# Performance work log

Measured on AMD Instinct MI355X. Metric: run time of the kernel, lower is better.

The kernel has to match this reference:

```python
import jax, jax.numpy as jnp
import numpy as np

_FP8_DTYPE = jnp.float8_e4m3fn
_FP8_MAX = 448.0  # finfo(float8_e4m3fn).max


def setup_inputs() -> dict:
    key = jax.random.key(0)
    k_x, k_w = jax.random.split(key)
    B, S, IN, OUT = 2, 8192, 2048, 2048
    x = jax.random.normal(k_x, (B, S, IN), dtype=jnp.float32)
    # weight stored in fp8_e4m3fn, per-tensor scalar weight_scale
    w_f32 = jax.random.normal(k_w, (OUT, IN), dtype=jnp.float32) * 0.02
    weight = w_f32.astype(_FP8_DTYPE)
    weight_scale = jnp.asarray(1.5, dtype=jnp.float32)
    input_scale = jnp.asarray(0.75, dtype=jnp.bfloat16)  # bf16 buffer as in torch
    return {"x": x, "weight": weight, "weight_scale": weight_scale, "input_scale": input_scale}


def reference(x, weight, weight_scale, input_scale):
    orig_dtype = x.dtype
    # dequantize fp8 weight: w = fp8 * scale (in original dtype)
    w = weight.astype(orig_dtype) * weight_scale.astype(orig_dtype)
    # static fake-quant of activations: scale -> clamp -> fp8 cast -> dequant
    s_f32 = input_scale.astype(jnp.float32)
    x_scaled = x.astype(jnp.float32) / s_f32
    x_fp8 = jnp.clip(x_scaled, -_FP8_MAX, _FP8_MAX).astype(_FP8_DTYPE)
    x_qdq = x_fp8.astype(orig_dtype) * s_f32.astype(orig_dtype)
    # dense linear: [B,S,IN] @ [OUT,IN]^T -> [B,S,OUT]
    return jnp.einsum("bsi,oi->bso", x_qdq, w)
```

## Files before the change

kernel.cpp:

```cpp
#include <hip/hip_runtime.h>
#include <hip/hip_bf16.h>
#include <stdint.h>

#define M_DIM 16384
#define N_DIM 2048
#define K_DIM 2048

typedef float    f32x4 __attribute__((ext_vector_type(4)));
typedef uint32_t u32x4 __attribute__((ext_vector_type(4)));
typedef int      i32x8 __attribute__((ext_vector_type(8)));

#define SCALE_ONE 0x7F7F7F7F

__device__ inline uint32_t quant4(float4 v, float rs) {
    float q0 = fminf(fmaxf(v.x * rs, -448.f), 448.f);
    float q1 = fminf(fmaxf(v.y * rs, -448.f), 448.f);
    float q2 = fminf(fmaxf(v.z * rs, -448.f), 448.f);
    float q3 = fminf(fmaxf(v.w * rs, -448.f), 448.f);
    int p = __builtin_amdgcn_cvt_pk_fp8_f32(q0, q1, 0, false);
    p     = __builtin_amdgcn_cvt_pk_fp8_f32(q2, q3, p, true);
    return (uint32_t)p;
}

__global__ __launch_bounds__(256) void quant_xw_kernel(
    const float* __restrict__ x, const float* __restrict__ w,
    const float* __restrict__ s_ptr,
    uint32_t* __restrict__ xq, uint32_t* __restrict__ wq)
{
    if (blockIdx.x < 2048) {
        const float rs = 1.0f / s_ptr[0];
        const float4* xf4 = (const float4*)x;
        const int base = blockIdx.x * 4096 + threadIdx.x;
#pragma unroll
        for (int k = 0; k < 16; ++k) {
            const int i = base + k * 256;
            xq[i] = quant4(xf4[i], rs);
        }
    } else {
        const float4* wf4 = (const float4*)w;
        const int base = (blockIdx.x - 2048) * 1024 + threadIdx.x;
#pragma unroll
        for (int k = 0; k < 4; ++k) {
            const int i = base + k * 256;
            wq[i] = quant4(wf4[i], 1.0f);
        }
    }
}

#define G_BM 256
#define G_BN 256
#define G_NT 16
#define G_GM (M_DIM / G_BM)
#define G_GN (N_DIM / G_BN)
#define SLOT 65536

extern __shared__ uint8_t smem[];

__global__ __launch_bounds__(512, 1) void gemm_mx_256sq(
    const uint8_t* __restrict__ Aq,
    const uint8_t* __restrict__ Wq,
    const float* __restrict__ wscale,
    const float* __restrict__ iscale,
    float* __restrict__ out)
{
    const int tid  = threadIdx.x;
    const int lane = tid & 63;
    const int wid  = tid >> 6;

    const int bid = blockIdx.x;
    const int wg  = (bid & 7) * (G_GM * G_GN / 8) + (bid >> 3);
    const int bm  = wg >> 3;
    const int bn  = wg & 7;
    const int rowBase = bm * G_BM;
    const int colBase = bn * G_BN;

    const int wrow = (wid >> 2) * 128;
    const int wcol = (wid & 3) * 64;

    const float scv = wscale[0] * iscale[0];

    const int sposx = (((lane & 7) ^ (lane >> 3)) * 16);
    const uint8_t* gA0 = Aq + (size_t)(rowBase + (tid >> 3)) * K_DIM + sposx;
    const uint8_t* gB0 = Wq + (size_t)(colBase + (tid >> 3)) * K_DIM + sposx;
    const int ldsW = wid * 1024;

    auto stage = [&](int buf, int tt) {
        const size_t koff = (size_t)tt * 128;
        uint8_t* sb = smem + buf * SLOT;
#pragma unroll
        for (int i = 0; i < 4; ++i)
            __builtin_amdgcn_global_load_lds(
                (const __attribute__((address_space(1))) void*)(gA0 + (size_t)i * (64 * K_DIM) + koff),
                (__attribute__((address_space(3))) void*)(sb + i * 8192 + ldsW),
                16, 0, 0);
#pragma unroll
        for (int i = 0; i < 4; ++i)
            __builtin_amdgcn_global_load_lds(
                (const __attribute__((address_space(1))) void*)(gB0 + (size_t)i * (64 * K_DIM) + koff),
                (__attribute__((address_space(3))) void*)(sb + 32768 + i * 8192 + ldsW),
                16, 0, 0);
    };

    const int fr  = lane & 15;
    const int rx  = fr & 7;
    const int pLo = (((lane >> 4) * 2) ^ rx) * 16;

    f32x4 acc[8][4] = {};

    stage(0, 0);
    __syncthreads();

    for (int t = 0; t < G_NT; ++t) {
        const int cur = t & 1;
        if (t + 1 < G_NT) stage(cur ^ 1, t + 1);

        const uint8_t* sb = smem + cur * SLOT;

        i32x8 bv[4];
#pragma unroll
        for (int n = 0; n < 4; ++n) {
            const int ro = 32768 + (wcol + n * 16 + fr) * 128;
            u32x4 lo = *(const u32x4*)(sb + ro + pLo);
            u32x4 hi = *(const u32x4*)(sb + ro + (pLo ^ 16));
            bv[n] = (i32x8){(int)lo.x, (int)lo.y, (int)lo.z, (int)lo.w,
                            (int)hi.x, (int)hi.y, (int)hi.z, (int)hi.w};
        }
#pragma unroll
        for (int m = 0; m < 8; ++m) {
            const int ro = (wrow + m * 16 + fr) * 128;
            u32x4 lo = *(const u32x4*)(sb + ro + pLo);
            u32x4 hi = *(const u32x4*)(sb + ro + (pLo ^ 16));
            const i32x8 av = {(int)lo.x, (int)lo.y, (int)lo.z, (int)lo.w,
                              (int)hi.x, (int)hi.y, (int)hi.z, (int)hi.w};
#pragma unroll
            for (int n = 0; n < 4; ++n)
                acc[m][n] = __builtin_amdgcn_mfma_scale_f32_16x16x128_f8f6f4(
                    av, bv[n], acc[m][n], 0, 0, 0, SCALE_ONE, 0, SCALE_ONE);
        }
        __syncthreads();
    }

    const int crow = (lane >> 4) << 2;
    const int ccol = lane & 15;
#pragma unroll
    for (int m = 0; m < 8; ++m) {
#pragma unroll
        for (int n = 0; n < 4; ++n) {
            const size_t base = (size_t)(rowBase + wrow + m * 16 + crow) * N_DIM
                              + (colBase + wcol + n * 16 + ccol);
#pragma unroll
            for (int r = 0; r < 4; ++r)
                out[base + (size_t)r * N_DIM] = acc[m][n][r] * scv;
        }
    }
}

__global__ __launch_bounds__(256) void fused_fp8_gemm(
    const float* __restrict__ X, const float* __restrict__ Wf,
    const float* __restrict__ wscale, const float* __restrict__ iscale,
    float* __restrict__ out)
{
    __shared__ uint8_t smA[2][128 * 64];
    __shared__ uint8_t smB[2][128 * 64];

    const int tid  = threadIdx.x;
    const int lane = tid & 63;
    const int wid  = tid >> 6;

    const float s  = iscale[0];
    const float rs = 1.0f / s;
    const float sc = wscale[0] * s;

    const int bid = blockIdx.x;
    const int wg  = (bid & 7) * 256 + (bid >> 3);
    const int bm  = wg >> 4;
    const int bn  = wg & 15;
    const int rowBase = bm * 128;
    const int colBase = bn * 128;
    const int wrow = (wid >> 1) * 64;
    const int wcol = (wid & 1) * 64;
    const int ar = tid >> 1;
    const int ah = (tid & 1) * 32;

    const float* Xrow = X  + (size_t)(rowBase + ar) * K_DIM;
    const float* Wrow = Wf + (size_t)(colBase + ar) * K_DIM;

    float4 areg[8], breg[8];
    auto load_tile = [&](int kt) {
        const int k0 = kt * 64;
#pragma unroll
        for (int j = 0; j < 8; ++j) areg[j] = *(const float4*)(Xrow + k0 + ah + j * 4);
#pragma unroll
        for (int j = 0; j < 8; ++j) breg[j] = *(const float4*)(Wrow + k0 + ah + j * 4);
    };
    auto write_tile = [&](int buf) {
        uint32_t aq[8], bq[8];
#pragma unroll
        for (int j = 0; j < 8; ++j) { aq[j] = quant4(areg[j], rs); bq[j] = quant4(breg[j], 1.0f); }
        *(u32x4*)&smA[buf][ar * 64 + ah]      = *(const u32x4*)&aq[0];
        *(u32x4*)&smA[buf][ar * 64 + ah + 16] = *(const u32x4*)&aq[4];
        *(u32x4*)&smB[buf][ar * 64 + ah]      = *(const u32x4*)&bq[0];
        *(u32x4*)&smB[buf][ar * 64 + ah + 16] = *(const u32x4*)&bq[4];
    };

    f32x4 acc[4][4] = {};
    load_tile(0); write_tile(0); __syncthreads();
    for (int kt = 0; kt < 32; ++kt) {
        const int cur = kt & 1;
        if (kt + 1 < 32) load_tile(kt + 1);
        const uint8_t* pA = smA[cur];
        const uint8_t* pB = smB[cur];
        const int afr = lane & 15, koff = (lane >> 4) << 3;
#pragma unroll
        for (int kk = 0; kk < 2; ++kk) {
            long long a[4], b[4];
#pragma unroll
            for (int m = 0; m < 4; ++m)
                a[m] = *(const long long*)(pA + (wrow + m * 16 + afr) * 64 + kk * 32 + koff);
#pragma unroll
            for (int n = 0; n < 4; ++n)
                b[n] = *(const long long*)(pB + (wcol + n * 16 + afr) * 64 + kk * 32 + koff);
#pragma unroll
            for (int m = 0; m < 4; ++m)
#pragma unroll
                for (int n = 0; n < 4; ++n)
                    acc[m][n] = __builtin_amdgcn_mfma_f32_16x16x32_fp8_fp8(
                        a[m], b[n], acc[m][n], 0, 0, 0);
        }
        if (kt + 1 < 32) write_tile(cur ^ 1);
        __syncthreads();
    }
    const int crow = (lane >> 4) << 2, ccol = lane & 15;
#pragma unroll
    for (int m = 0; m < 4; ++m)
#pragma unroll
        for (int n = 0; n < 4; ++n) {
            const size_t base = (size_t)(rowBase + wrow + m * 16 + crow) * N_DIM
                              + (colBase + wcol + n * 16 + ccol);
#pragma unroll
            for (int r = 0; r < 4; ++r)
                out[base + (size_t)r * N_DIM] = acc[m][n][r] * sc;
        }
}

extern "C" void kernel_launch(void* const* d_in, const int* in_sizes, int n_in,
                              void* d_out, int out_size, void* d_ws, size_t ws_size,
                              hipStream_t stream) {
    const float* x      = (const float*)d_in[0];
    const float* w      = (const float*)d_in[1];
    const float* wscale = (const float*)d_in[2];
    const float* iscale = (const float*)d_in[3];
    float*       out    = (float*)d_out;

    const size_t needA = (size_t)M_DIM * K_DIM;
    const size_t needW = (size_t)N_DIM * K_DIM;

    hipError_t e = hipFuncSetAttribute((const void*)gemm_mx_256sq,
                                       hipFuncAttributeMaxDynamicSharedMemorySize,
                                       2 * SLOT);

    if (e == hipSuccess && ws_size >= needA + needW) {
        uint32_t* xq = (uint32_t*)d_ws;
        uint32_t* wq = (uint32_t*)((uint8_t*)d_ws + needA);
        quant_xw_kernel<<<3072, 256, 0, stream>>>(x, w, iscale, xq, wq);
        gemm_mx_256sq<<<G_GM * G_GN, 512, 2 * SLOT, stream>>>(
            (const uint8_t*)xq, (const uint8_t*)wq, wscale, iscale, out);
    } else {
        fused_fp8_gemm<<<2048, 256, 0, stream>>>(x, w, wscale, iscale, out);
    }
}
```

Before: 111.5 us.

## Split GEMM main loop into phased LDS-read/MFMA stages with explicit barriers

Restructures the K loop into four phases, each reading two A fragments from LDS and then issuing eight MFMAs. Raw s_barrier, explicit waitcnt, sched_barrier and s_setprio replace __syncthreads, in the style of a ping-pong schedule across the 8 waves. The next-tile global-to-LDS prefetch is now issued after the B and first A reads rather than before them. The aim is to interleave LDS traffic and matrix-core work across waves and to cut register pressure from holding all A fragments. The cost is many more barriers per iteration, which could serialise waves if the phases do not overlap.

```diff
diff --git a/kernel.cpp b/kernel.cpp
--- a/kernel.cpp
+++ b/kernel.cpp
@@ -56,7 +56,17 @@
 
 extern __shared__ uint8_t smem[];
 
-__global__ __launch_bounds__(512, 1) void gemm_mx_256sq(
+#define MFMA_PAIR(M0, M1, A0_, A1_)                                           \
+    _Pragma("unroll")                                                         \
+    for (int n = 0; n < 4; ++n)                                               \
+        acc[M0][n] = __builtin_amdgcn_mfma_scale_f32_16x16x128_f8f6f4(        \
+            A0_, bv[n], acc[M0][n], 0, 0, 0, SCALE_ONE, 0, SCALE_ONE);        \
+    _Pragma("unroll")                                                         \
+    for (int n = 0; n < 4; ++n)                                               \
+        acc[M1][n] = __builtin_amdgcn_mfma_scale_f32_16x16x128_f8f6f4(        \
+            A1_, bv[n], acc[M1][n], 0, 0, 0, SCALE_ONE, 0, SCALE_ONE);
+
+__global__ __launch_bounds__(512, 1) void gemm_mx_8ph(
     const uint8_t* __restrict__ Aq,
     const uint8_t* __restrict__ Wq,
     const float* __restrict__ wscale,
@@ -78,6 +88,7 @@
     const int wcol = (wid & 3) * 64;
 
     const float scv = wscale[0] * iscale[0];
+    asm volatile("" :: "v"(scv));
 
     const int sposx = (((lane & 7) ^ (lane >> 3)) * 16);
     const uint8_t* gA0 = Aq + (size_t)(rowBase + (tid >> 3)) * K_DIM + sposx;
@@ -102,42 +113,83 @@
     };
 
     const int fr  = lane & 15;
-    const int rx  = fr & 7;
-    const int pLo = (((lane >> 4) * 2) ^ rx) * 16;
+    const int pLo = (((lane >> 4) * 2) ^ (fr & 7)) * 16;
+
+    auto readA = [&](const uint8_t* sb, int m) -> i32x8 {
+        const int ro = (wrow + m * 16 + fr) * 128;
+        u32x4 lo = *(const u32x4*)(sb + ro + pLo);
+        u32x4 hi = *(const u32x4*)(sb + ro + (pLo ^ 16));
+        return (i32x8){(int)lo.x, (int)lo.y, (int)lo.z, (int)lo.w,
+                       (int)hi.x, (int)hi.y, (int)hi.z, (int)hi.w};
+    };
+    auto readB = [&](const uint8_t* sb, int n) -> i32x8 {
+        const int ro = 32768 + (wcol + n * 16 + fr) * 128;
+        u32x4 lo = *(const u32x4*)(sb + ro + pLo);
+        u32x4 hi = *(const u32x4*)(sb + ro + (pLo ^ 16));
+        return (i32x8){(int)lo.x, (int)lo.y, (int)lo.z, (int)lo.w,
+                       (int)hi.x, (int)hi.y, (int)hi.z, (int)hi.w};
+    };
 
     f32x4 acc[8][4] = {};
 
     stage(0, 0);
-    __syncthreads();
+    asm volatile("s_waitcnt vmcnt(0)" ::: "memory");
+    __builtin_amdgcn_s_barrier();
+    __builtin_amdgcn_sched_barrier(0);
 
     for (int t = 0; t < G_NT; ++t) {
         const int cur = t & 1;
+        const uint8_t* sb = smem + cur * SLOT;
+
+        i32x8 bv[4];
+#pragma unroll
+        for (int n = 0; n < 4; ++n) bv[n] = readB(sb, n);
+        i32x8 aE0 = readA(sb, 0), aE1 = readA(sb, 1);
         if (t + 1 < G_NT) stage(cur ^ 1, t + 1);
-
-        const uint8_t* sb = smem + cur * SLOT;
-
-        i32x8 bv[4];
-#pragma unroll
-        for (int n = 0; n < 4; ++n) {
-            const int ro = 32768 + (wcol + n * 16 + fr) * 128;
-            u32x4 lo = *(const u32x4*)(sb + ro + pLo);
-            u32x4 hi = *(const u32x4*)(sb + ro + (pLo ^ 16));
-            bv[n] = (i32x8){(int)lo.x, (int)lo.y, (int)lo.z, (int)lo.w,
-                            (int)hi.x, (int)hi.y, (int)hi.z, (int)hi.w};
-        }
-#pragma unroll
-        for (int m = 0; m < 8; ++m) {
-            const int ro = (wrow + m * 16 + fr) * 128;
-            u32x4 lo = *(const u32x4*)(sb + ro + pLo);
-            u32x4 hi = *(const u32x4*)(sb + ro + (pLo ^ 16));
-            const i32x8 av = {(int)lo.x, (int)lo.y, (int)lo.z, (int)lo.w,
-                              (int)hi.x, (int)hi.y, (int)hi.z, (int)hi.w};
-#pragma unroll
-            for (int n = 0; n < 4; ++n)
-                acc[m][n] = __builtin_amdgcn_mfma_scale_f32_16x16x128_f8f6f4(
-                    av, bv[n], acc[m][n], 0, 0, 0, SCALE_ONE, 0, SCALE_ONE);
-        }
-        __syncthreads();
+        __builtin_amdgcn_sched_barrier(0);
+        __builtin_amdgcn_s_barrier();
+        asm volatile("s_waitcnt lgkmcnt(0)" ::: "memory");
+        __builtin_amdgcn_sched_barrier(0);
+        __builtin_amdgcn_s_setprio(1);
+        MFMA_PAIR(0, 1, aE0, aE1)
+        __builtin_amdgcn_s_setprio(0);
+        __builtin_amdgcn_sched_barrier(0);
+        __builtin_amdgcn_s_barrier();
+
+        i32x8 aO0 = readA(sb, 2), aO1 = readA(sb, 3);
+        __builtin_amdgcn_sched_barrier(0);
+        __builtin_amdgcn_s_barrier();
+        asm volatile("s_waitcnt lgkmcnt(0)" ::: "memory");
+        __builtin_amdgcn_sched_barrier(0);
+        __builtin_amdgcn_s_setprio(1);
+        MFMA_PAIR(2, 3, aO0, aO1)
+        __builtin_amdgcn_s_setprio(0);
+        __builtin_amdgcn_sched_barrier(0);
+        __builtin_amdgcn_s_barrier();
+
+        aE0 = readA(sb, 4); aE1 = readA(sb, 5);
+        __builtin_amdgcn_sched_barrier(0);
+        __builtin_amdgcn_s_barrier();
+        asm volatile("s_waitcnt lgkmcnt(0)" ::: "memory");
+        __builtin_amdgcn_sched_barrier(0);
+        __builtin_amdgcn_s_setprio(1);
+        MFMA_PAIR(4, 5, aE0, aE1)
+        __builtin_amdgcn_s_setprio(0);
+        __builtin_amdgcn_sched_barrier(0);
+        __builtin_amdgcn_s_barrier();
+
+        aO0 = readA(sb, 6); aO1 = readA(sb, 7);
+        __builtin_amdgcn_sched_barrier(0);
+        __builtin_amdgcn_s_barrier();
+        asm volatile("s_waitcnt lgkmcnt(0)" ::: "memory");
+        __builtin_amdgcn_sched_barrier(0);
+        __builtin_amdgcn_s_setprio(1);
+        MFMA_PAIR(6, 7, aO0, aO1)
+        __builtin_amdgcn_s_setprio(0);
+        __builtin_amdgcn_sched_barrier(0);
+        asm volatile("s_waitcnt vmcnt(0)" ::: "memory");
+        __builtin_amdgcn_s_barrier();
+        __builtin_amdgcn_sched_barrier(0);
     }
 
     const int crow = (lane >> 4) << 2;
@@ -255,7 +307,7 @@
     const size_t needA = (size_t)M_DIM * K_DIM;
     const size_t needW = (size_t)N_DIM * K_DIM;
 
-    hipError_t e = hipFuncSetAttribute((const void*)gemm_mx_256sq,
+    hipError_t e = hipFuncSetAttribute((const void*)gemm_mx_8ph,
                                        hipFuncAttributeMaxDynamicSharedMemorySize,
                                        2 * SLOT);
 
@@ -263,7 +315,7 @@
         uint32_t* xq = (uint32_t*)d_ws;
         uint32_t* wq = (uint32_t*)((uint8_t*)d_ws + needA);
         quant_xw_kernel<<<3072, 256, 0, stream>>>(x, w, iscale, xq, wq);
-        gemm_mx_256sq<<<G_GM * G_GN, 512, 2 * SLOT, stream>>>(
+        gemm_mx_8ph<<<G_GM * G_GN, 512, 2 * SLOT, stream>>>(
             (const uint8_t*)xq, (const uint8_t*)wq, wscale, iscale, out);
     } else {
         fused_fp8_gemm<<<2048, 256, 0, stream>>>(x, w, wscale, iscale, out);
```

New measurement: 119.4 us. 1.07x slower.

## Drop LDS double buffering and raise launch-bounds occupancy target for GEMM

Applied to the files above, without the earlier changes.

The FP8 MX GEMM kernel now uses a single 64KB LDS slot instead of two. Each k-tile is loaded and then synchronised before compute, so global-to-LDS loads no longer overlap MFMA work. The launch bounds go from 1 to 4 blocks per CU so that more workgroups can be resident and hide latency through occupancy instead of software pipelining. The higher occupancy hint caps registers per thread, which could force spills of the 128-float accumulator, and the serialised load/compute adds exposed latency.

```diff
diff --git a/kernel.cpp b/kernel.cpp
--- a/kernel.cpp
+++ b/kernel.cpp
@@ -56,7 +56,7 @@
 
 extern __shared__ uint8_t smem[];
 
-__global__ __launch_bounds__(512, 1) void gemm_mx_256sq(
+__global__ __launch_bounds__(512, 4) void gemm_mx_sb(
     const uint8_t* __restrict__ Aq,
     const uint8_t* __restrict__ Wq,
     const float* __restrict__ wscale,
@@ -84,52 +84,45 @@
     const uint8_t* gB0 = Wq + (size_t)(colBase + (tid >> 3)) * K_DIM + sposx;
     const int ldsW = wid * 1024;
 
-    auto stage = [&](int buf, int tt) {
+    auto stage = [&](int tt) {
         const size_t koff = (size_t)tt * 128;
-        uint8_t* sb = smem + buf * SLOT;
 #pragma unroll
         for (int i = 0; i < 4; ++i)
             __builtin_amdgcn_global_load_lds(
                 (const __attribute__((address_space(1))) void*)(gA0 + (size_t)i * (64 * K_DIM) + koff),
-                (__attribute__((address_space(3))) void*)(sb + i * 8192 + ldsW),
+                (__attribute__((address_space(3))) void*)(smem + i * 8192 + ldsW),
                 16, 0, 0);
 #pragma unroll
         for (int i = 0; i < 4; ++i)
             __builtin_amdgcn_global_load_lds(
                 (const __attribute__((address_space(1))) void*)(gB0 + (size_t)i * (64 * K_DIM) + koff),
-                (__attribute__((address_space(3))) void*)(sb + 32768 + i * 8192 + ldsW),
+                (__attribute__((address_space(3))) void*)(smem + 32768 + i * 8192 + ldsW),
                 16, 0, 0);
     };
 
     const int fr  = lane & 15;
-    const int rx  = fr & 7;
-    const int pLo = (((lane >> 4) * 2) ^ rx) * 16;
+    const int pLo = (((lane >> 4) * 2) ^ (fr & 7)) * 16;
 
     f32x4 acc[8][4] = {};
 
-    stage(0, 0);
-    __syncthreads();
-
     for (int t = 0; t < G_NT; ++t) {
-        const int cur = t & 1;
-        if (t + 1 < G_NT) stage(cur ^ 1, t + 1);
-
-        const uint8_t* sb = smem + cur * SLOT;
+        stage(t);
+        __syncthreads();
 
         i32x8 bv[4];
 #pragma unroll
         for (int n = 0; n < 4; ++n) {
             const int ro = 32768 + (wcol + n * 16 + fr) * 128;
-            u32x4 lo = *(const u32x4*)(sb + ro + pLo);
-            u32x4 hi = *(const u32x4*)(sb + ro + (pLo ^ 16));
+            u32x4 lo = *(const u32x4*)(smem + ro + pLo);
+            u32x4 hi = *(const u32x4*)(smem + ro + (pLo ^ 16));
             bv[n] = (i32x8){(int)lo.x, (int)lo.y, (int)lo.z, (int)lo.w,
                             (int)hi.x, (int)hi.y, (int)hi.z, (int)hi.w};
         }
 #pragma unroll
         for (int m = 0; m < 8; ++m) {
             const int ro = (wrow + m * 16 + fr) * 128;
-            u32x4 lo = *(const u32x4*)(sb + ro + pLo);
-            u32x4 hi = *(const u32x4*)(sb + ro + (pLo ^ 16));
+            u32x4 lo = *(const u32x4*)(smem + ro + pLo);
+            u32x4 hi = *(const u32x4*)(smem + ro + (pLo ^ 16));
             const i32x8 av = {(int)lo.x, (int)lo.y, (int)lo.z, (int)lo.w,
                               (int)hi.x, (int)hi.y, (int)hi.z, (int)hi.w};
 #pragma unroll
@@ -255,15 +248,15 @@
     const size_t needA = (size_t)M_DIM * K_DIM;
     const size_t needW = (size_t)N_DIM * K_DIM;
 
-    hipError_t e = hipFuncSetAttribute((const void*)gemm_mx_256sq,
+    hipError_t e = hipFuncSetAttribute((const void*)gemm_mx_sb,
                                        hipFuncAttributeMaxDynamicSharedMemorySize,
-                                       2 * SLOT);
+                                       SLOT);
 
     if (e == hipSuccess && ws_size >= needA + needW) {
         uint32_t* xq = (uint32_t*)d_ws;
         uint32_t* wq = (uint32_t*)((uint8_t*)d_ws + needA);
         quant_xw_kernel<<<3072, 256, 0, stream>>>(x, w, iscale, xq, wq);
-        gemm_mx_256sq<<<G_GM * G_GN, 512, 2 * SLOT, stream>>>(
+        gemm_mx_sb<<<G_GM * G_GN, 512, SLOT, stream>>>(
             (const uint8_t*)xq, (const uint8_t*)wq, wscale, iscale, out);
     } else {
         fused_fp8_gemm<<<2048, 256, 0, stream>>>(x, w, wscale, iscale, out);
```

Result: slower. 368.4 us (+230.3%).

## Load A operand directly from global memory into registers, stage only B in LDS

Applied to the files above, without the earlier changes.

The GEMM kernel no longer stages the quantized activation tile in shared memory. Each wave reads its A fragments straight from global memory inside the k-loop, and only the weight tile is double-buffered via global_load_lds. This halves LDS usage, and with the min-blocks launch bound removed it may allow higher occupancy. The cost is that A rows are re-read by several waves from cache, and the global loads are issued without prefetch, so their latency sits on the critical path.

```diff
diff --git a/kernel.cpp b/kernel.cpp
--- a/kernel.cpp
+++ b/kernel.cpp
@@ -52,11 +52,11 @@
 #define G_NT 16
 #define G_GM (M_DIM / G_BM)
 #define G_GN (N_DIM / G_BN)
-#define SLOT 65536
+#define BSLOT 32768
 
 extern __shared__ uint8_t smem[];
 
-__global__ __launch_bounds__(512, 1) void gemm_mx_256sq(
+__global__ __launch_bounds__(512) void gemm_mx_adir(
     const uint8_t* __restrict__ Aq,
     const uint8_t* __restrict__ Wq,
     const float* __restrict__ wscale,
@@ -80,56 +80,52 @@
     const float scv = wscale[0] * iscale[0];
 
     const int sposx = (((lane & 7) ^ (lane >> 3)) * 16);
-    const uint8_t* gA0 = Aq + (size_t)(rowBase + (tid >> 3)) * K_DIM + sposx;
     const uint8_t* gB0 = Wq + (size_t)(colBase + (tid >> 3)) * K_DIM + sposx;
     const int ldsW = wid * 1024;
 
-    auto stage = [&](int buf, int tt) {
+    auto stageB = [&](int buf, int tt) {
         const size_t koff = (size_t)tt * 128;
-        uint8_t* sb = smem + buf * SLOT;
-#pragma unroll
-        for (int i = 0; i < 4; ++i)
-            __builtin_amdgcn_global_load_lds(
-                (const __attribute__((address_space(1))) void*)(gA0 + (size_t)i * (64 * K_DIM) + koff),
-                (__attribute__((address_space(3))) void*)(sb + i * 8192 + ldsW),
-                16, 0, 0);
+        uint8_t* sb = smem + buf * BSLOT;
 #pragma unroll
         for (int i = 0; i < 4; ++i)
             __builtin_amdgcn_global_load_lds(
                 (const __attribute__((address_space(1))) void*)(gB0 + (size_t)i * (64 * K_DIM) + koff),
-                (__attribute__((address_space(3))) void*)(sb + 32768 + i * 8192 + ldsW),
+                (__attribute__((address_space(3))) void*)(sb + i * 8192 + ldsW),
                 16, 0, 0);
     };
 
     const int fr  = lane & 15;
-    const int rx  = fr & 7;
-    const int pLo = (((lane >> 4) * 2) ^ rx) * 16;
+    const int pLo = (((lane >> 4) * 2) ^ (fr & 7)) * 16;
+
+    const uint8_t* gA = Aq + (size_t)(rowBase + wrow + fr) * K_DIM + (lane >> 4) * 32;
 
     f32x4 acc[8][4] = {};
 
-    stage(0, 0);
+    stageB(0, 0);
     __syncthreads();
 
     for (int t = 0; t < G_NT; ++t) {
         const int cur = t & 1;
-        if (t + 1 < G_NT) stage(cur ^ 1, t + 1);
-
-        const uint8_t* sb = smem + cur * SLOT;
+        if (t + 1 < G_NT) stageB(cur ^ 1, t + 1);
+
+        const uint8_t* sb = smem + cur * BSLOT;
 
         i32x8 bv[4];
 #pragma unroll
         for (int n = 0; n < 4; ++n) {
-            const int ro = 32768 + (wcol + n * 16 + fr) * 128;
+            const int ro = (wcol + n * 16 + fr) * 128;
             u32x4 lo = *(const u32x4*)(sb + ro + pLo);
             u32x4 hi = *(const u32x4*)(sb + ro + (pLo ^ 16));
             bv[n] = (i32x8){(int)lo.x, (int)lo.y, (int)lo.z, (int)lo.w,
                             (int)hi.x, (int)hi.y, (int)hi.z, (int)hi.w};
         }
+
+        const uint8_t* gAt = gA + t * 128;
 #pragma unroll
         for (int m = 0; m < 8; ++m) {
-            const int ro = (wrow + m * 16 + fr) * 128;
-            u32x4 lo = *(const u32x4*)(sb + ro + pLo);
-            u32x4 hi = *(const u32x4*)(sb + ro + (pLo ^ 16));
+            const uint8_t* p = gAt + (size_t)m * (16 * K_DIM);
+            u32x4 lo = *(const u32x4*)(p);
+            u32x4 hi = *(const u32x4*)(p + 16);
             const i32x8 av = {(int)lo.x, (int)lo.y, (int)lo.z, (int)lo.w,
                               (int)hi.x, (int)hi.y, (int)hi.z, (int)hi.w};
 #pragma unroll
@@ -255,15 +251,15 @@
     const size_t needA = (size_t)M_DIM * K_DIM;
     const size_t needW = (size_t)N_DIM * K_DIM;
 
-    hipError_t e = hipFuncSetAttribute((const void*)gemm_mx_256sq,
+    hipError_t e = hipFuncSetAttribute((const void*)gemm_mx_adir,
                                        hipFuncAttributeMaxDynamicSharedMemorySize,
-                                       2 * SLOT);
+                                       2 * BSLOT);
 
     if (e == hipSuccess && ws_size >= needA + needW) {
         uint32_t* xq = (uint32_t*)d_ws;
         uint32_t* wq = (uint32_t*)((uint8_t*)d_ws + needA);
         quant_xw_kernel<<<3072, 256, 0, stream>>>(x, w, iscale, xq, wq);
-        gemm_mx_256sq<<<G_GM * G_GN, 512, 2 * SLOT, stream>>>(
+        gemm_mx_adir<<<G_GM * G_GN, 512, 2 * BSLOT, stream>>>(
             (const uint8_t*)xq, (const uint8_t*)wq, wscale, iscale, out);
     } else {
         fused_fp8_gemm<<<2048, 256, 0, stream>>>(x, w, wscale, iscale, out);
```

New measurement: 182.0 us. 1.63x slower.
